# Kernel optimization log

Hardware: AMD Instinct MI355X
Metric: run time of the kernel (lower is better)

## Reference

```python
import jax, jax.numpy as jnp
import numpy as np
import math

E = 2048; H = 16; NOPE = 128; ROPE = 64; VH = 128; C = 512; QR = 1536
DR = 2; BASE = 10000.0; LR = 4  # hypernet low_rank -> C//4 = 128
B = 2; S = 2048


def _ln(x, g, b):
    m = jnp.mean(x, axis=-1, keepdims=True)
    v = jnp.mean((x - m) ** 2, axis=-1, keepdims=True)
    return (x - m) / jnp.sqrt(v + 1e-5) * g + b


def _rope(x, sin, cos):
    # interleaved rotary: x[..., 0::2], x[..., 1::2]
    x1 = x[..., 0::2]
    x2 = x[..., 1::2]
    out = jnp.stack([x1 * cos - x2 * sin, x1 * sin + x2 * cos], axis=-1)
    return out.reshape(x.shape)


def _sincos(pos, dim):
    inv = BASE ** (-jnp.arange(0, dim, 2, dtype=jnp.float32) / dim)
    ang = pos[:, None] * inv  # [S, dim//2]
    return jnp.sin(ang), jnp.cos(ang)


def _pe(T, d):
    # sinusoidal positional encoding [T, d]
    pos = jnp.arange(T, dtype=jnp.float32)[:, None]
    div = jnp.exp(jnp.arange(0, d, 2, dtype=jnp.float32) * (-math.log(10000.0) / d))
    pe = jnp.zeros((T, d))
    pe = pe.at[:, 0::2].set(jnp.sin(pos * div))
    pe = pe.at[:, 1::2].set(jnp.cos(pos * div))
    return pe


def _forward(query, key, value, wq_a, q_ln_g, q_ln_b, wq_b, wkv_a, kv_ln_g,
             kv_ln_b, wkv_b, wo, fc_c_w, fc_c_b, fc_p_w, fc_p_b, pos_scale):
    B_, S_, _ = query.shape
    # LoRA query path
    ql = _ln(query @ wq_a.T, q_ln_g, q_ln_b)                 # [B,S,QR]
    q = (ql @ wq_b.T).reshape(B_, S_, H, NOPE + ROPE)
    q_nope, q_pe = q[..., :NOPE], q[..., NOPE:]
    # positions: start_pos = key_len - 1 (prefill entering incremental path)
    start = S_ - 1
    pos = jnp.arange(start, start + S_, dtype=jnp.float32)
    sin, cos = _sincos(pos, ROPE)                            # [S, ROPE//2]
    q_pe = _rope(q_pe, sin[None, :, None, :], cos[None, :, None, :])
    # KV latent path
    kvf = key @ wkv_a.T                                      # [B,S,C+ROPE]
    kv, k_pe = kvf[..., :C], kvf[..., C:]
    k_pe = _rope(k_pe, sin[None, :, :], cos[None, :, :])     # [B,S,ROPE]
    kvn = _ln(kv, kv_ln_g, kv_ln_b)                          # [B,S,C]
    # HyperNetwork temporal compression: W [B, t, T]
    T = S_
    t = math.ceil(T / DR)
    Cpe = _pe(t, C)                                          # [t, C]
    C2 = Cpe @ fc_c_w.T + fc_c_b                             # [t, C//LR]
    P2 = kvn @ fc_p_w.T + fc_p_b                             # [B,T,C//LR]
    W = jax.nn.sigmoid(jnp.einsum('tr,bTr->btT', C2, P2))    # [B,t,T]
    # chunk mask: compressed slot r gathers tokens in its down_rate chunk
    zm = (jnp.arange(T)[None, :] // DR == jnp.arange(t)[:, None]).astype(kvn.dtype)
    prev_kv = jnp.einsum('btT,bTc->btc', W * zm[None], kvn)  # [B,t,C]
    idx = list(range(DR - 1, T, DR))
    if T - 1 not in idx:
        idx.append(T - 1)
    prev_kpe = k_pe[:, np.array(idx)]                        # [B,t,ROPE]
    # LoRA-absorbed attention
    wkvb = wkv_b.reshape(H, NOPE + VH, C)
    qn = jnp.einsum('bshd,hdc->bshc', q_nope, wkvb[:, :NOPE])
    content = jnp.einsum('bshc,btc->bsht', qn, prev_kv)
    # decoupled (normalized) rope scores
    qpe_n = q_pe / jnp.maximum(jnp.linalg.norm(q_pe, axis=-1, keepdims=True), 1e-12)
    kpe_n = prev_kpe / jnp.maximum(jnp.linalg.norm(prev_kpe, axis=-1, keepdims=True), 1e-12)
    pscore = jnp.einsum('bshr,btr->bsht', qpe_n, kpe_n)
    scores = (content + pos_scale * pscore) * ((NOPE + ROPE) ** -0.5)
    attn = jax.nn.softmax(scores, axis=-1)                   # [B,S,H,t]
    x = jnp.einsum('bsht,btc->bshc', attn, prev_kv)
    x = jnp.einsum('bshc,hdc->bshd', x, wkvb[:, NOPE:])      # value up-proj
    return x.reshape(B_, S_, H * VH) @ wo.T


def setup_inputs() -> dict:
    key = jax.random.key(0)
    ks = jax.random.split(key, 16)
    s = 0.02
    return {
        'query': jax.random.normal(ks[0], (B, S, E), jnp.float32),
        'key': jax.random.normal(ks[1], (B, S, E), jnp.float32),
        'value': jax.random.normal(ks[2], (B, S, E), jnp.float32),
        'wq_a': jax.random.normal(ks[3], (QR, E), jnp.float32) * s,
        'q_ln_g': jnp.ones((QR,), jnp.float32),
        'q_ln_b': jnp.zeros((QR,), jnp.float32),
        'wq_b': jax.random.normal(ks[4], (H * (NOPE + ROPE), QR), jnp.float32) * s,
        'wkv_a': jax.random.normal(ks[5], (C + ROPE, E), jnp.float32) * s,
        'kv_ln_g': jnp.ones((C,), jnp.float32),
        'kv_ln_b': jnp.zeros((C,), jnp.float32),
        'wkv_b': jax.random.normal(ks[6], (H * (NOPE + VH), C), jnp.float32) * s,
        'wo': jax.random.normal(ks[7], (E, H * VH), jnp.float32) * s,
        'fc_c_w': jax.random.normal(ks[8], (C // LR, C), jnp.float32) * s,
        'fc_c_b': jnp.zeros((C // LR,), jnp.float32),
        'fc_p_w': jax.random.normal(ks[9], (C // LR, C), jnp.float32) * s,
        'fc_p_b': jnp.zeros((C // LR,), jnp.float32),
        'pos_scale': jnp.asarray(1.0, jnp.float32),
    }


def reference(query, key, value, wq_a, q_ln_g, q_ln_b, wq_b, wkv_a, kv_ln_g,
              kv_ln_b, wkv_b, wo, fc_c_w, fc_c_b, fc_p_w, fc_p_b, pos_scale):
    return _forward(query, key, value, wq_a, q_ln_g, q_ln_b, wq_b, wkv_a,
                    kv_ln_g, kv_ln_b, wkv_b, wo, fc_c_w, fc_c_b, fc_p_w,
                    fc_p_b, pos_scale)
```

## Files before the change

### kernel.cpp

```cpp
#include <hip/hip_runtime.h>
#include <math.h>

#define S_ 2048
#define B_ 2
#define H_ 16
#define E_ 2048
#define QR_ 1536
#define NOPE_ 128
#define ROPE_ 64
#define C_ 512
#define VH_ 128
#define T_ 1024
#define LN1E4 9.210340371976184f
#define SCALE_ 0.07216878364870323f

typedef _Float16 half8 __attribute__((ext_vector_type(8)));
typedef _Float16 half4 __attribute__((ext_vector_type(4)));
typedef __fp16 fp16x2 __attribute__((ext_vector_type(2)));
typedef float floatx4 __attribute__((ext_vector_type(4)));
#define MFMA16(a, b, c) __builtin_amdgcn_mfma_f32_16x16x32_f16(a, b, c, 0, 0, 0)

__device__ __forceinline__ void gload16(const _Float16* g, _Float16* l) {
  __builtin_amdgcn_global_load_lds(
      (__attribute__((address_space(1))) const void*)g,
      (__attribute__((address_space(3))) void*)l, 16, 0, 0);
}

__device__ __forceinline__ int xcd_swizzle(int orig, int nwg) {
  int q8 = nwg >> 3, r8 = nwg & 7, xcd = orig & 7, base = orig >> 3;
  return (xcd < r8 ? xcd * (q8 + 1) : r8 * (q8 + 1) + (xcd - r8) * q8) + base;
}

__global__ __launch_bounds__(256) void conv_all(
    const float* __restrict__ q, const float* __restrict__ k,
    const float* __restrict__ wqa, const float* __restrict__ wqb,
    const float* __restrict__ wkva, const float* __restrict__ wo,
    const float* __restrict__ fcc, const float* __restrict__ fcp,
    const float* __restrict__ wkvb,
    _Float16* q16, _Float16* k16, _Float16* wqa16, _Float16* wqb16,
    _Float16* wkva16, _Float16* wo16, _Float16* fcc16, _Float16* fcp16,
    _Float16* W1c, _Float16* W2c)
{
  size_t i = (size_t)blockIdx.x * 256 + threadIdx.x;
  if (i >= 3768320) {
    bool isW1 = i < 3899392;
    size_t j = i - (isW1 ? 3768320 : 3899392);
    int cch = j & 63, hd = (int)(j >> 6);
    int hh = hd >> 7, dd = hd & 127;
    const float* src = wkvb + ((size_t)(hh * 256 + (isW1 ? 0 : 128) + dd)) * 512 + cch * 8;
    float sc = isW1 ? SCALE_ : 1.f;
    float4 a = *(const float4*)src;
    float4 b = *(const float4*)(src + 4);
    half8 h = {(_Float16)(a.x * sc), (_Float16)(a.y * sc), (_Float16)(a.z * sc),
               (_Float16)(a.w * sc), (_Float16)(b.x * sc), (_Float16)(b.y * sc),
               (_Float16)(b.z * sc), (_Float16)(b.w * sc)};
    *(half8*)((isW1 ? W1c : W2c) + j * 8) = h;
    return;
  }
  const float* in; _Float16* out; size_t off;
  if      (i < 1048576) { in = q;    out = q16;    off = i; }
  else if (i < 2097152) { in = k;    out = k16;    off = i - 1048576; }
  else if (i < 2490368) { in = wqa;  out = wqa16;  off = i - 2097152; }
  else if (i < 3080192) { in = wqb;  out = wqb16;  off = i - 2490368; }
  else if (i < 3227648) { in = wkva; out = wkva16; off = i - 3080192; }
  else if (i < 3751936) { in = wo;   out = wo16;   off = i - 3227648; }
  else if (i < 3760128) { in = fcc;  out = fcc16;  off = i - 3751936; }
  else                  { in = fcp;  out = fcp16;  off = i - 3760128; }
  float4 a = ((const float4*)in)[2 * off];
  float4 b = ((const float4*)in)[2 * off + 1];
  half8 h = {(_Float16)a.x, (_Float16)a.y, (_Float16)a.z, (_Float16)a.w,
             (_Float16)b.x, (_Float16)b.y, (_Float16)b.z, (_Float16)b.w};
  *(half8*)(out + 8 * off) = h;
}

template<bool OUT16, bool NB, bool BIAS, bool TRANSC, bool DUAL = false>
__global__ __launch_bounds__(256) void gemm16(
    const _Float16* __restrict__ A, const _Float16* __restrict__ Bm,
    const float* __restrict__ bias, const float* __restrict__ bias2,
    float* __restrict__ Cf, _Float16* __restrict__ Ch,
    int N, int K, int lda, int ldb, int ldc,
    long sAb, long sAh, long sBb, long sBh, long sCb, long sCh)
{
  __shared__ __align__(16) _Float16 Asl[2][128 * 64];
  __shared__ __align__(16) _Float16 Bsl[2][128 * 64];
  int mode = 0;
  if (DUAL) {
    int zz = blockIdx.z;
    mode = zz >> 5;
    int z2 = zz & 31;
    int zb2 = z2 >> 4, zh2 = z2 & 15;
    A += (size_t)zb2 * sAb;
    const _Float16* Bsel = mode ? (const _Float16*)bias2 : Bm;
    Bm = Bsel + (size_t)zh2 * (128 * C_);
    if (mode) Ch = ((_Float16*)Cf) + ((size_t)(zb2 * H_ + zh2) * 128) * T_;
    else      Ch += ((size_t)(zb2 * H_ + zh2) * T_) * 192;
  } else {
    const int z = blockIdx.z, zb = z >> 4, zh = z & 15;
    A  += (size_t)zb * sAb + (size_t)zh * sAh;
    Bm += (size_t)zb * sBb + (size_t)zh * sBh;
    if (OUT16) Ch += (size_t)zb * sCb + (size_t)zh * sCh;
    else       Cf += (size_t)zb * sCb + (size_t)zh * sCh;
  }
  const int gx = gridDim.x;
  const int nwg = gx * gridDim.y;
  const int f = xcd_swizzle(blockIdx.y * gx + blockIdx.x, nwg);
  const int bm = (f / gx) * 128, bn = (f % gx) * 128;
  const int tid = threadIdx.x;
  const int w = tid >> 6, lane = tid & 63, l15 = lane & 15, g = lane >> 4;
  const int wm = (w >> 1) * 64, wn = (w & 1) * 64;
  const int srow = w * 32 + (lane >> 3);
  const int sch  = (lane & 7) ^ (lane >> 3);
  floatx4 acc[4][4];
  #pragma unroll
  for (int i = 0; i < 4; ++i)
    #pragma unroll
    for (int j = 0; j < 4; ++j) acc[i][j] = (floatx4){0.f, 0.f, 0.f, 0.f};

  auto STAGE = [&](int buf, int k0) {
    _Float16* al = &Asl[buf][w * 2048];
    _Float16* bl = &Bsl[buf][w * 2048];
    #pragma unroll
    for (int i = 0; i < 4; ++i)
      gload16(A + (size_t)(bm + srow + i * 8) * lda + k0 + sch * 8, al + i * 512);
    #pragma unroll
    for (int i = 0; i < 4; ++i)
      gload16(Bm + (size_t)(bn + srow + i * 8) * ldb + k0 + sch * 8, bl + i * 512);
  };

  STAGE(0, 0);
  int cur = 0;
  const int nIter = K >> 6;
  for (int it = 0; it < nIter; ++it) {
    const bool pf = (it + 1 < nIter);
    if (pf) STAGE(cur ^ 1, (it + 1) << 6);
    if (pf) asm volatile("s_waitcnt vmcnt(8)" ::: "memory");
    else    asm volatile("s_waitcnt vmcnt(0)" ::: "memory");
    __builtin_amdgcn_sched_barrier(0);
    __builtin_amdgcn_s_barrier();
    __builtin_amdgcn_sched_barrier(0);
    #pragma unroll
    for (int kk = 0; kk < 2; ++kk) {
      half8 af[4], bf[4];
      const int sw = ((kk * 4 + g) ^ (l15 & 7)) * 8;
      #pragma unroll
      for (int i = 0; i < 4; ++i) {
        af[i] = *(const half8*)&Asl[cur][(wm + i * 16 + l15) * 64 + sw];
        bf[i] = *(const half8*)&Bsl[cur][(wn + i * 16 + l15) * 64 + sw];
      }
      #pragma unroll
      for (int i = 0; i < 4; ++i)
        #pragma unroll
        for (int j = 0; j < 4; ++j)
          acc[i][j] = MFMA16(af[i], bf[j], acc[i][j]);
    }
    asm volatile("s_waitcnt lgkmcnt(0)" ::: "memory");
    __builtin_amdgcn_sched_barrier(0);
    __builtin_amdgcn_s_barrier();
    __builtin_amdgcn_sched_barrier(0);
    cur ^= 1;
  }

  if (DUAL) {
    if (mode) {
      #pragma unroll
      for (int i = 0; i < 4; ++i)
        #pragma unroll
        for (int j = 0; j < 4; ++j) {
          int row = bm + wm + i * 16 + g * 4;
          int col = wn + j * 16 + l15;
          half4 v = {(_Float16)acc[i][j][0], (_Float16)acc[i][j][1],
                     (_Float16)acc[i][j][2], (_Float16)acc[i][j][3]};
          *(half4*)(Ch + (size_t)col * T_ + row) = v;
        }
    } else {
      #pragma unroll
      for (int i = 0; i < 4; ++i)
        #pragma unroll
        for (int j = 0; j < 4; ++j)
          #pragma unroll
          for (int r = 0; r < 4; ++r) {
            int row = bm + wm + i * 16 + g * 4 + r;
            int col = wn + j * 16 + l15;
            Ch[(size_t)row * 192 + col] = (_Float16)acc[i][j][r];
          }
    }
  } else if (TRANSC) {
    #pragma unroll
    for (int i = 0; i < 4; ++i)
      #pragma unroll
      for (int j = 0; j < 4; ++j) {
        int row = bm + wm + i * 16 + g * 4;
        int col = bn + wn + j * 16 + l15;
        half4 v = {(_Float16)acc[i][j][0], (_Float16)acc[i][j][1],
                   (_Float16)acc[i][j][2], (_Float16)acc[i][j][3]};
        *(half4*)(Ch + (size_t)col * ldc + row) = v;
      }
  } else {
    #pragma unroll
    for (int i = 0; i < 4; ++i)
      #pragma unroll
      for (int j = 0; j < 4; ++j)
        #pragma unroll
        for (int r = 0; r < 4; ++r) {
          int row = bm + wm + i * 16 + g * 4 + r;
          int col = bn + wn + j * 16 + l15;
          if (!NB || col < N) {
            float v = acc[i][j][r];
            if (BIAS) v += (col < 128) ? bias[col] : bias2[col - 128];
            if (OUT16) Ch[(size_t)row * ldc + col] = (_Float16)v;
            else       Cf[(size_t)row * ldc + col] = v;
          }
        }
  }
}

struct GTask {
  const _Float16* A; const _Float16* B; _Float16* C;
  const float* b1; const float* b2;
  int gx, N, K, lda, ldb, ldc;
};

__global__ __launch_bounds__(256) void gemm_pair(GTask ta, GTask tb, int n0, int n1)
{
  __shared__ __align__(16) _Float16 Asl[2][128 * 64];
  __shared__ __align__(16) _Float16 Bsl[2][128 * 64];
  const bool second = blockIdx.x >= (unsigned)n0;
  GTask t = second ? tb : ta;
  const int fid = second ? blockIdx.x - n0 : blockIdx.x;
  const int nwg = second ? n1 : n0;
  const int f = xcd_swizzle(fid, nwg);
  const int bm = (f / t.gx) * 128, bn = (f % t.gx) * 128;
  const int tid = threadIdx.x;
  const int w = tid >> 6, lane = tid & 63, l15 = lane & 15, g = lane >> 4;
  const int wm = (w >> 1) * 64, wn = (w & 1) * 64;
  const int srow = w * 32 + (lane >> 3);
  const int sch  = (lane & 7) ^ (lane >> 3);
  floatx4 acc[4][4];
  #pragma unroll
  for (int i = 0; i < 4; ++i)
    #pragma unroll
    for (int j = 0; j < 4; ++j) acc[i][j] = (floatx4){0.f, 0.f, 0.f, 0.f};

  auto STAGE = [&](int buf, int k0) {
    _Float16* al = &Asl[buf][w * 2048];
    _Float16* bl = &Bsl[buf][w * 2048];
    #pragma unroll
    for (int i = 0; i < 4; ++i)
      gload16(t.A + (size_t)(bm + srow + i * 8) * t.lda + k0 + sch * 8, al + i * 512);
    #pragma unroll
    for (int i = 0; i < 4; ++i)
      gload16(t.B + (size_t)(bn + srow + i * 8) * t.ldb + k0 + sch * 8, bl + i * 512);
  };

  STAGE(0, 0);
  int cur = 0;
  const int nIter = t.K >> 6;
  for (int it = 0; it < nIter; ++it) {
    const bool pf = (it + 1 < nIter);
    if (pf) STAGE(cur ^ 1, (it + 1) << 6);
    if (pf) asm volatile("s_waitcnt vmcnt(8)" ::: "memory");
    else    asm volatile("s_waitcnt vmcnt(0)" ::: "memory");
    __builtin_amdgcn_sched_barrier(0);
    __builtin_amdgcn_s_barrier();
    __builtin_amdgcn_sched_barrier(0);
    #pragma unroll
    for (int kk = 0; kk < 2; ++kk) {
      half8 af[4], bf[4];
      const int sw = ((kk * 4 + g) ^ (l15 & 7)) * 8;
      #pragma unroll
      for (int i = 0; i < 4; ++i) {
        af[i] = *(const half8*)&Asl[cur][(wm + i * 16 + l15) * 64 + sw];
        bf[i] = *(const half8*)&Bsl[cur][(wn + i * 16 + l15) * 64 + sw];
      }
      #pragma unroll
      for (int i = 0; i < 4; ++i)
        #pragma unroll
        for (int j = 0; j < 4; ++j)
          acc[i][j] = MFMA16(af[i], bf[j], acc[i][j]);
    }
    asm volatile("s_waitcnt lgkmcnt(0)" ::: "memory");
    __builtin_amdgcn_sched_barrier(0);
    __builtin_amdgcn_s_barrier();
    __builtin_amdgcn_sched_barrier(0);
    cur ^= 1;
  }
  #pragma unroll
  for (int i = 0; i < 4; ++i)
    #pragma unroll
    for (int j = 0; j < 4; ++j)
      #pragma unroll
      for (int r = 0; r < 4; ++r) {
        int row = bm + wm + i * 16 + g * 4 + r;
        int col = bn + wn + j * 16 + l15;
        if (col < t.N) {
          float v = acc[i][j][r];
          if (t.b1) v += (col < 128) ? t.b1[col] : t.b2[col - 128];
          t.C[(size_t)row * t.ldc + col] = (_Float16)v;
        }
      }
}

__global__ __launch_bounds__(256) void fused_ln(
    _Float16* __restrict__ ql16, const _Float16* __restrict__ kvf16,
    _Float16* __restrict__ kvnA,
    const float* __restrict__ qg, const float* __restrict__ qb,
    const float* __restrict__ kg, const float* __restrict__ kb,
    _Float16* __restrict__ keff, _Float16* __restrict__ Cpe16)
{
  __shared__ float rs[4], rs2[4];
  int bid = blockIdx.x;
  const int tid = threadIdx.x;
  const int lane = tid & 63, w = tid >> 6;
  if (bid < 8192) {
    const bool isQ = bid < 4096;
    const int row = isQ ? bid : bid - 4096;
    const _Float16* x = isQ ? ql16 + (size_t)row * 1536 : kvf16 + (size_t)row * 576;
    _Float16* o = isQ ? ql16 + (size_t)row * 1536 : kvnA + (size_t)row * 512;
    const float* g_ = isQ ? qg : kg;
    const float* b_ = isQ ? qb : kb;
    const int L = isQ ? 1536 : 512;
    float s = 0.f, s2 = 0.f;
    for (int i = tid; i < L; i += 256) {
      float v = (float)x[i]; s += v; s2 += v * v;
    }
    #pragma unroll
    for (int off = 32; off; off >>= 1) {
      s  += __shfl_xor(s, off, 64);
      s2 += __shfl_xor(s2, off, 64);
    }
    if (lane == 0) { rs[w] = s; rs2[w] = s2; }
    __syncthreads();
    s  = rs[0] + rs[1] + rs[2] + rs[3];
    s2 = rs2[0] + rs2[1] + rs2[2] + rs2[3];
    float mean = s / L;
    float var = s2 / L - mean * mean;
    float inv = rsqrtf(var + 1e-5f);
    for (int i = tid; i < L; i += 256)
      o[i] = (_Float16)(((float)x[i] - mean) * inv * g_[i] + b_[i]);
    return;
  }
  bid -= 8192;
  if (bid < 512) {
    int u = bid * 4 + w;
    int t = u & (T_ - 1), b = u >> 10;
    const int srow = 2 * t + 1;
    const _Float16* p = kvf16 + ((size_t)(b * S_ + srow)) * 576 + C_;
    float o1 = 0.f, o2 = 0.f;
    if (lane < 32) {
      float invf = expf(-(float)lane * (LN1E4 / 32.f));
      float ang = (float)(S_ - 1 + srow) * invf;
      float sn, cs; sincosf(ang, &sn, &cs);
      float x1 = (float)p[2 * lane], x2 = (float)p[2 * lane + 1];
      o1 = x1 * cs - x2 * sn;
      o2 = x1 * sn + x2 * cs;
    }
    float ss = o1 * o1 + o2 * o2;
    #pragma unroll
    for (int off = 32; off; off >>= 1) ss += __shfl_xor(ss, off, 64);
    float nrm = fmaxf(sqrtf(ss), 1e-12f);
    if (lane < 32) {
      _Float16 h1 = (_Float16)(o1 / nrm), h2 = (_Float16)(o2 / nrm);
      #pragma unroll
      for (int h = 0; h < H_; ++h) {
        _Float16* o = keff + ((size_t)((b * H_ + h) * T_) + t) * 192 + NOPE_;
        o[2 * lane] = h1; o[2 * lane + 1] = h2;
      }
    }
    return;
  }
  bid -= 512;
  {
    const int t = bid;
    float dv = expf(-(float)(2 * tid) * (LN1E4 / 512.f));
    float ang = (float)t * dv;
    float sn, cs; sincosf(ang, &sn, &cs);
    Cpe16[(size_t)t * C_ + 2 * tid]     = (_Float16)sn;
    Cpe16[(size_t)t * C_ + 2 * tid + 1] = (_Float16)cs;
  }
}

__global__ __launch_bounds__(256) void fused_rq_gate(
    _Float16* __restrict__ qb16, const float* __restrict__ ps_ptr,
    const _Float16* __restrict__ Ccat, const _Float16* __restrict__ kvnA,
    _Float16* __restrict__ pkv16)
{
  int bid = blockIdx.x;
  const int tid = threadIdx.x;
  const int lane = tid & 63, w = tid >> 6;
  if (bid < 4096) {
    const int row = bid;
    const int s = row & (S_ - 1);
    float sn = 0.f, cs = 0.f;
    if (lane < 32) {
      float invf = expf(-(float)lane * (LN1E4 / 32.f));
      float ang = (float)(S_ - 1 + s) * invf;
      sincosf(ang, &sn, &cs);
    }
    const float psc = ps_ptr[0] * SCALE_;
    #pragma unroll
    for (int hh = 0; hh < 4; ++hh) {
      const int h = w + hh * 4;
      _Float16* p = qb16 + (size_t)row * 3072 + h * 192 + NOPE_;
      float o1 = 0.f, o2 = 0.f;
      if (lane < 32) {
        float x1 = (float)p[2 * lane], x2 = (float)p[2 * lane + 1];
        o1 = x1 * cs - x2 * sn;
        o2 = x1 * sn + x2 * cs;
      }
      float ss = o1 * o1 + o2 * o2;
      #pragma unroll
      for (int off = 32; off; off >>= 1) ss += __shfl_xor(ss, off, 64);
      float inv = psc / fmaxf(sqrtf(ss), 1e-12f);
      if (lane < 32) {
        p[2 * lane]     = (_Float16)(o1 * inv);
        p[2 * lane + 1] = (_Float16)(o2 * inv);
      }
    }
    return;
  }
  bid -= 4096;
  {
    int u = bid * 4 + w;
    int t = u & (T_ - 1), b = u >> 10;
    const int j = lane;
    const _Float16* c2 = Ccat + (size_t)t * 256;
    const _Float16* p0 = Ccat + (size_t)(1024 + b * S_ + 2 * t) * 256 + 128;
    const _Float16* p1 = p0 + 256;
    float d0 = (float)c2[j] * (float)p0[j] + (float)c2[j + 64] * (float)p0[j + 64];
    float d1 = (float)c2[j] * (float)p1[j] + (float)c2[j + 64] * (float)p1[j + 64];
    #pragma unroll
    for (int off = 32; off; off >>= 1) {
      d0 += __shfl_xor(d0, off, 64);
      d1 += __shfl_xor(d1, off, 64);
    }
    float w0 = 1.f / (1.f + expf(-d0));
    float w1 = 1.f / (1.f + expf(-d1));
    const _Float16* k0 = kvnA + ((size_t)(b * S_ + 2 * t)) * C_;
    const _Float16* k1 = k0 + C_;
    _Float16* o = pkv16 + ((size_t)(b * T_ + t)) * C_;
    #pragma unroll
    for (int it = 0; it < 2; ++it) {
      int c = j * 4 + it * 256;
      half4 a = *(const half4*)(k0 + c);
      half4 bb = *(const half4*)(k1 + c);
      half4 r;
      #pragma unroll
      for (int uu = 0; uu < 4; ++uu)
        r[uu] = (_Float16)(w0 * (float)a[uu] + w1 * (float)bb[uu]);
      *(half4*)(o + c) = r;
    }
  }
}

__global__ __launch_bounds__(256, 2) void attn_flash(
    const _Float16* __restrict__ qb16, const _Float16* __restrict__ keff,
    const _Float16* __restrict__ vT, _Float16* __restrict__ x216)
{
  __shared__ __align__(16) _Float16 K_lds[2][64 * 192];
  __shared__ __align__(16) _Float16 V_lds[2][128 * 64];
  const int f = xcd_swizzle(blockIdx.x, 1024);
  const int st = f & 31, h = (f >> 5) & 15, b = f >> 9;
  const int tid = threadIdx.x, w = tid >> 6, lane = tid & 63;
  const int l15 = lane & 15, g = lane >> 4, l7 = lane & 7;
  const int rq = b * S_ + st * 64 + w * 16;
  const _Float16* qrow = qb16 + (size_t)(rq + l15) * 3072 + h * 192;
  half8 qB[6];
  #pragma unroll
  for (int kk = 0; kk < 6; ++kk) qB[kk] = *(const half8*)(qrow + kk * 32 + g * 8);
  floatx4 O[8];
  #pragma unroll
  for (int i = 0; i < 8; ++i) O[i] = (floatx4){0.f, 0.f, 0.f, 0.f};
  float m = -3e38f, l = 0.f;
  const _Float16* kb = keff + (size_t)(b * H_ + h) * T_ * 192;
  const _Float16* vb = vT   + (size_t)(b * H_ + h) * 128 * T_;

  int ksrc[6], ksw[6], vsrc[4], vsw[4];
  #pragma unroll
  for (int p = 0; p < 6; ++p) {
    int c = tid + p * 256;
    int r = c / 24, dc = c % 24;
    ksrc[p] = r * 192 + dc * 8;
    ksw[p]  = r * 192 + ((dc ^ (r & 7)) * 8);
  }
  #pragma unroll
  for (int p = 0; p < 4; ++p) {
    int c = tid + p * 256;
    int r = c >> 3, dc = c & 7;
    vsrc[p] = r * T_ + dc * 8;
    vsw[p]  = r * 64 + ((dc ^ (r & 7)) * 8);
  }
  int kswr[6], vswr[2];
  #pragma unroll
  for (int kk = 0; kk < 6; ++kk) kswr[kk] = ((kk * 4 + g) ^ l7) * 8;
  #pragma unroll
  for (int kc = 0; kc < 2; ++kc) vswr[kc] = ((kc * 4 + g) ^ l7) * 8;

  half8 kreg[6], vreg[4];
  #pragma unroll
  for (int p = 0; p < 6; ++p) kreg[p] = *(const half8*)(kb + ksrc[p]);
  #pragma unroll
  for (int p = 0; p < 4; ++p) vreg[p] = *(const half8*)(vb + vsrc[p]);
  #pragma unroll
  for (int p = 0; p < 6; ++p) *(half8*)&K_lds[0][ksw[p]] = kreg[p];
  #pragma unroll
  for (int p = 0; p < 4; ++p) *(half8*)&V_lds[0][vsw[p]] = vreg[p];
  __syncthreads();

  const int srcA = l15 + ((g & 1) << 5);
  const int srcB = srcA + 16;
  const bool hi = (g >> 1) != 0;

  int cur = 0;
  for (int kt = 0; kt < 16; ++kt) {
    if (kt < 15) {
      const int t1 = (kt + 1) * 64;
      #pragma unroll
      for (int p = 0; p < 6; ++p)
        kreg[p] = *(const half8*)(kb + (size_t)t1 * 192 + ksrc[p]);
      #pragma unroll
      for (int p = 0; p < 4; ++p)
        vreg[p] = *(const half8*)(vb + t1 + vsrc[p]);
    }
    floatx4 sc[4];
    #pragma unroll
    for (int i = 0; i < 4; ++i) sc[i] = (floatx4){0.f, 0.f, 0.f, 0.f};
    __builtin_amdgcn_s_setprio(1);
    #pragma unroll
    for (int kk = 0; kk < 6; ++kk)
      #pragma unroll
      for (int ct = 0; ct < 4; ++ct)
        sc[ct] = MFMA16(
            *(const half8*)&K_lds[cur][(ct * 16 + l15) * 192 + kswr[kk]],
            qB[kk], sc[ct]);
    __builtin_amdgcn_s_setprio(0);
    float pm = sc[0][0];
    #pragma unroll
    for (int ct = 0; ct < 4; ++ct)
      #pragma unroll
      for (int r = 0; r < 4; ++r) pm = fmaxf(pm, sc[ct][r]);
    pm = fmaxf(pm, __shfl_xor(pm, 16, 64));
    pm = fmaxf(pm, __shfl_xor(pm, 32, 64));
    int ok = pm <= m + 8.f;
    if (!__all(ok)) {
      float mn = fmaxf(m, pm);
      float sf = __expf(m - mn);
      m = mn; l *= sf;
      float sfO[4];
      #pragma unroll
      for (int r = 0; r < 4; ++r) sfO[r] = __shfl(sf, g * 4 + r, 64);
      #pragma unroll
      for (int cc = 0; cc < 8; ++cc) {
        O[cc][0] *= sfO[0]; O[cc][1] *= sfO[1];
        O[cc][2] *= sfO[2]; O[cc][3] *= sfO[3];
      }
    }
    float rs = 0.f;
    #pragma unroll
    for (int ct = 0; ct < 4; ++ct)
      #pragma unroll
      for (int r = 0; r < 4; ++r) {
        float e = __expf(sc[ct][r] - m);
        sc[ct][r] = e; rs += e;
      }
    rs += __shfl_xor(rs, 16, 64);
    rs += __shfl_xor(rs, 32, 64);
    l += rs;
    unsigned pk[4][2];
    #pragma unroll
    for (int ct = 0; ct < 4; ++ct) {
      union { fp16x2 h; unsigned u; } c0, c1;
      c0.h = __builtin_amdgcn_cvt_pkrtz(sc[ct][0], sc[ct][1]);
      c1.h = __builtin_amdgcn_cvt_pkrtz(sc[ct][2], sc[ct][3]);
      pk[ct][0] = c0.u; pk[ct][1] = c1.u;
    }
    __builtin_amdgcn_s_setprio(1);
    #pragma unroll
    for (int kc = 0; kc < 2; ++kc) {
      unsigned a0 = __shfl((int)pk[2 * kc][0], srcA, 64);
      unsigned b0 = __shfl((int)pk[2 * kc + 1][0], srcA, 64);
      unsigned a1 = __shfl((int)pk[2 * kc][1], srcA, 64);
      unsigned b1 = __shfl((int)pk[2 * kc + 1][1], srcA, 64);
      unsigned a2 = __shfl((int)pk[2 * kc][0], srcB, 64);
      unsigned b2 = __shfl((int)pk[2 * kc + 1][0], srcB, 64);
      unsigned a3 = __shfl((int)pk[2 * kc][1], srcB, 64);
      unsigned b3 = __shfl((int)pk[2 * kc + 1][1], srcB, 64);
      union { unsigned u[4]; half8 h; } pa;
      pa.u[0] = hi ? b0 : a0;
      pa.u[1] = hi ? b1 : a1;
      pa.u[2] = hi ? b2 : a2;
      pa.u[3] = hi ? b3 : a3;
      #pragma unroll
      for (int cc = 0; cc < 8; ++cc)
        O[cc] = MFMA16(pa.h,
            *(const half8*)&V_lds[cur][(cc * 16 + l15) * 64 + vswr[kc]], O[cc]);
    }
    __builtin_amdgcn_s_setprio(0);
    if (kt < 15) {
      #pragma unroll
      for (int p = 0; p < 6; ++p) *(half8*)&K_lds[cur ^ 1][ksw[p]] = kreg[p];
      #pragma unroll
      for (int p = 0; p < 4; ++p) *(half8*)&V_lds[cur ^ 1][vsw[p]] = vreg[p];
      __syncthreads();
      cur ^= 1;
    }
  }
  float il = 1.f / l;
  float ilO[4];
  #pragma unroll
  for (int r = 0; r < 4; ++r) ilO[r] = __shfl(il, g * 4 + r, 64);
  #pragma unroll
  for (int cc = 0; cc < 8; ++cc)
    #pragma unroll
    for (int r = 0; r < 4; ++r)
      x216[(size_t)(rq + g * 4 + r) * 2048 + h * 128 + cc * 16 + l15] =
          (_Float16)(O[cc][r] * ilO[r]);
}

extern "C" void kernel_launch(void* const* d_in, const int* in_sizes, int n_in,
                              void* d_out, int out_size, void* d_ws, size_t ws_size,
                              hipStream_t stream)
{
  (void)in_sizes; (void)n_in; (void)out_size; (void)ws_size;
  const float* query  = (const float*)d_in[0];
  const float* key    = (const float*)d_in[1];
  const float* wq_a   = (const float*)d_in[3];
  const float* q_ln_g = (const float*)d_in[4];
  const float* q_ln_b = (const float*)d_in[5];
  const float* wq_b   = (const float*)d_in[6];
  const float* wkv_a  = (const float*)d_in[7];
  const float* kv_ln_g= (const float*)d_in[8];
  const float* kv_ln_b= (const float*)d_in[9];
  const float* wkvb   = (const float*)d_in[10];
  const float* wo     = (const float*)d_in[11];
  const float* fc_c_w = (const float*)d_in[12];
  const float* fc_c_b = (const float*)d_in[13];
  const float* fc_p_w = (const float*)d_in[14];
  const float* fc_p_b = (const float*)d_in[15];
  const float* ps     = (const float*)d_in[16];
  float* out = (float*)d_out;

  const int M = B_ * S_;
  _Float16* hws   = (_Float16*)d_ws;
  _Float16* q16   = hws;
  _Float16* key16 = q16   + (size_t)8388608;
  _Float16* wqa16 = key16 + (size_t)8388608;
  _Float16* wqb16 = wqa16 + (size_t)3145728;
  _Float16* wkva16= wqb16 + (size_t)4718592;
  _Float16* wo16  = wkva16+ (size_t)1179648;
  _Float16* ql16  = wo16  + (size_t)4194304;
  _Float16* qb16  = ql16  + (size_t)6291456;
  _Float16* kvf16 = qb16  + (size_t)12582912;
  _Float16* kvn16 = kvf16 + (size_t)2359296;
  _Float16* fcc16 = kvn16 + (size_t)2097152;
  _Float16* fcp16 = fcc16 + (size_t)65536;
  _Float16* W1c   = fcp16 + (size_t)65536;
  _Float16* W2c   = W1c   + (size_t)1048576;
  _Float16* x216  = q16;
  _Float16* keff  = key16;
  _Float16* Cpe16 = q16;
  _Float16* kvnA  = q16 + (size_t)524288;
  _Float16* Ccat  = wqa16;
  _Float16* pkv16 = wkva16;
  _Float16* vT    = ql16;

  conv_all<<<15744, 256, 0, stream>>>(query, key, wq_a, wq_b, wkv_a, wo, fc_c_w, fc_p_w,
                                      wkvb, q16, key16, wqa16, wqb16, wkva16, wo16,
                                      fcc16, fcp16, W1c, W2c);
  {
    GTask ta = {q16,   wqa16,  ql16,  nullptr, nullptr, 12, QR_, E_, E_, E_, QR_};
    GTask tb = {key16, wkva16, kvf16, nullptr, nullptr, 5,  576, E_, E_, E_, 576};
    gemm_pair<<<544, 256, 0, stream>>>(ta, tb, 384, 160);
  }
  fused_ln<<<9728, 256, 0, stream>>>(ql16, kvf16, kvnA, q_ln_g, q_ln_b,
                                     kv_ln_g, kv_ln_b, keff, Cpe16);
  {
    GTask ta = {ql16,  wqb16, qb16, nullptr, nullptr, 24, 3072, QR_, QR_, QR_, 3072};
    GTask tb = {Cpe16, fcc16, Ccat, fc_c_b,  fc_p_b,  2,  256,  C_,  C_,  C_,  256};
    gemm_pair<<<848, 256, 0, stream>>>(ta, tb, 768, 80);
  }
  fused_rq_gate<<<4608, 256, 0, stream>>>(qb16, ps, Ccat, kvnA, pkv16);
  gemm16<true,false,false,false,true><<<dim3(1, T_/128, 64), 256, 0, stream>>>(
      pkv16, W1c, nullptr, (const float*)W2c, (float*)vT, keff,
      128, C_, C_, C_, 192, (long)T_*C_, 0L, 0L, 0L, 0L, 0L);
  attn_flash<<<dim3(1024), 256, 0, stream>>>(qb16, keff, vT, x216);
  gemm16<false,false,false,false><<<dim3(E_/128, M/128), 256, 0, stream>>>(
      x216, wo16, nullptr, nullptr, out, nullptr, E_, E_, E_, E_, E_, 0,0,0,0,0,0);
}
```

Measured before the change: 322.1 us.

## Overlap deferred weight conversions with first GEMM pair launch

Splits the fp32-to-fp16 conversion kernel so only the inputs needed by the first GEMM pair (query, key, wq_a, wkv_a) are converted up front. The remaining weight conversions (wq_b, wo, fc weights, wkv_b split/scale) are appended as extra blocks to the first gemm_pair launch, so they can run on CUs left idle by the 544 GEMM tiles. The aim is to shorten the serial conversion phase and fill the GEMM's underutilized GPU. The cost is a larger grid and a branch in the GEMM kernel. The conversion blocks also share the kernel's LDS allocation, which may limit how many of them run at once.

```diff
diff --git a/kernel.cpp b/kernel.cpp
--- a/kernel.cpp
+++ b/kernel.cpp
@@ -31,41 +31,17 @@
   return (xcd < r8 ? xcd * (q8 + 1) : r8 * (q8 + 1) + (xcd - r8) * q8) + base;
 }
 
-__global__ __launch_bounds__(256) void conv_all(
+__global__ __launch_bounds__(256) void conv_a(
     const float* __restrict__ q, const float* __restrict__ k,
-    const float* __restrict__ wqa, const float* __restrict__ wqb,
-    const float* __restrict__ wkva, const float* __restrict__ wo,
-    const float* __restrict__ fcc, const float* __restrict__ fcp,
-    const float* __restrict__ wkvb,
-    _Float16* q16, _Float16* k16, _Float16* wqa16, _Float16* wqb16,
-    _Float16* wkva16, _Float16* wo16, _Float16* fcc16, _Float16* fcp16,
-    _Float16* W1c, _Float16* W2c)
+    const float* __restrict__ wqa, const float* __restrict__ wkva,
+    _Float16* q16, _Float16* k16, _Float16* wqa16, _Float16* wkva16)
 {
   size_t i = (size_t)blockIdx.x * 256 + threadIdx.x;
-  if (i >= 3768320) {
-    bool isW1 = i < 3899392;
-    size_t j = i - (isW1 ? 3768320 : 3899392);
-    int cch = j & 63, hd = (int)(j >> 6);
-    int hh = hd >> 7, dd = hd & 127;
-    const float* src = wkvb + ((size_t)(hh * 256 + (isW1 ? 0 : 128) + dd)) * 512 + cch * 8;
-    float sc = isW1 ? SCALE_ : 1.f;
-    float4 a = *(const float4*)src;
-    float4 b = *(const float4*)(src + 4);
-    half8 h = {(_Float16)(a.x * sc), (_Float16)(a.y * sc), (_Float16)(a.z * sc),
-               (_Float16)(a.w * sc), (_Float16)(b.x * sc), (_Float16)(b.y * sc),
-               (_Float16)(b.z * sc), (_Float16)(b.w * sc)};
-    *(half8*)((isW1 ? W1c : W2c) + j * 8) = h;
-    return;
-  }
   const float* in; _Float16* out; size_t off;
   if      (i < 1048576) { in = q;    out = q16;    off = i; }
   else if (i < 2097152) { in = k;    out = k16;    off = i - 1048576; }
   else if (i < 2490368) { in = wqa;  out = wqa16;  off = i - 2097152; }
-  else if (i < 3080192) { in = wqb;  out = wqb16;  off = i - 2490368; }
-  else if (i < 3227648) { in = wkva; out = wkva16; off = i - 3080192; }
-  else if (i < 3751936) { in = wo;   out = wo16;   off = i - 3227648; }
-  else if (i < 3760128) { in = fcc;  out = fcc16;  off = i - 3751936; }
-  else                  { in = fcp;  out = fcp16;  off = i - 3760128; }
+  else                  { in = wkva; out = wkva16; off = i - 2490368; }
   float4 a = ((const float4*)in)[2 * off];
   float4 b = ((const float4*)in)[2 * off + 1];
   half8 h = {(_Float16)a.x, (_Float16)a.y, (_Float16)a.z, (_Float16)a.w,
@@ -219,12 +195,51 @@
   const float* b1; const float* b2;
   int gx, N, K, lda, ldb, ldc;
 };
-
-__global__ __launch_bounds__(256) void gemm_pair(GTask ta, GTask tb, int n0, int n1)
+struct CTask {
+  const float* wqb; const float* wo; const float* fcc; const float* fcp;
+  const float* wkvb;
+  _Float16* wqb16; _Float16* wo16; _Float16* fcc16; _Float16* fcp16;
+  _Float16* W1c; _Float16* W2c;
+};
+
+__global__ __launch_bounds__(256) void gemm_pair(GTask ta, GTask tb, CTask tc,
+                                                 int n0, int n1)
 {
   __shared__ __align__(16) _Float16 Asl[2][128 * 64];
   __shared__ __align__(16) _Float16 Bsl[2][128 * 64];
-  const bool second = blockIdx.x >= (unsigned)n0;
+  if ((int)blockIdx.x >= n0 + n1) {
+    size_t j = (size_t)(blockIdx.x - n0 - n1) * 256 + threadIdx.x;
+    const float* in; _Float16* out; size_t off; float sc = 1.f;
+    if (j < 589824)       { in = tc.wqb; out = tc.wqb16; off = j; }
+    else if (j < 1114112) { in = tc.wo;  out = tc.wo16;  off = j - 589824; }
+    else if (j < 1122304) { in = tc.fcc; out = tc.fcc16; off = j - 1114112; }
+    else if (j < 1130496) { in = tc.fcp; out = tc.fcp16; off = j - 1122304; }
+    else {
+      size_t j2 = j - 1130496;
+      bool isW1 = j2 < 131072;
+      size_t jj = isW1 ? j2 : j2 - 131072;
+      int cch = jj & 63, hd = (int)(jj >> 6);
+      int hh = hd >> 7, dd = hd & 127;
+      in = tc.wkvb + ((size_t)(hh * 256 + (isW1 ? 0 : 128) + dd)) * 512 + cch * 8
+           - 0;
+      out = (isW1 ? tc.W1c : tc.W2c) + jj * 8;
+      sc = isW1 ? SCALE_ : 1.f;
+      float4 a = *(const float4*)in;
+      float4 b = *(const float4*)(in + 4);
+      half8 h = {(_Float16)(a.x * sc), (_Float16)(a.y * sc), (_Float16)(a.z * sc),
+                 (_Float16)(a.w * sc), (_Float16)(b.x * sc), (_Float16)(b.y * sc),
+                 (_Float16)(b.z * sc), (_Float16)(b.w * sc)};
+      *(half8*)out = h;
+      return;
+    }
+    float4 a = ((const float4*)in)[2 * off];
+    float4 b = ((const float4*)in)[2 * off + 1];
+    half8 h = {(_Float16)a.x, (_Float16)a.y, (_Float16)a.z, (_Float16)a.w,
+               (_Float16)b.x, (_Float16)b.y, (_Float16)b.z, (_Float16)b.w};
+    *(half8*)(out + 8 * off) = h;
+    return;
+  }
+  const bool second = (int)blockIdx.x >= n0;
   GTask t = second ? tb : ta;
   const int fid = second ? blockIdx.x - n0 : blockIdx.x;
   const int nwg = second ? n1 : n0;
@@ -663,20 +678,22 @@
   _Float16* pkv16 = wkva16;
   _Float16* vT    = ql16;
 
-  conv_all<<<15744, 256, 0, stream>>>(query, key, wq_a, wq_b, wkv_a, wo, fc_c_w, fc_p_w,
-                                      wkvb, q16, key16, wqa16, wqb16, wkva16, wo16,
-                                      fcc16, fcp16, W1c, W2c);
+  conv_a<<<10304, 256, 0, stream>>>(query, key, wq_a, wkv_a,
+                                    q16, key16, wqa16, wkva16);
   {
     GTask ta = {q16,   wqa16,  ql16,  nullptr, nullptr, 12, QR_, E_, E_, E_, QR_};
     GTask tb = {key16, wkva16, kvf16, nullptr, nullptr, 5,  576, E_, E_, E_, 576};
-    gemm_pair<<<544, 256, 0, stream>>>(ta, tb, 384, 160);
+    CTask tc = {wq_b, wo, fc_c_w, fc_p_w, wkvb,
+                wqb16, wo16, fcc16, fcp16, W1c, W2c};
+    gemm_pair<<<544 + 5440, 256, 0, stream>>>(ta, tb, tc, 384, 160);
   }
   fused_ln<<<9728, 256, 0, stream>>>(ql16, kvf16, kvnA, q_ln_g, q_ln_b,
                                      kv_ln_g, kv_ln_b, keff, Cpe16);
   {
     GTask ta = {ql16,  wqb16, qb16, nullptr, nullptr, 24, 3072, QR_, QR_, QR_, 3072};
     GTask tb = {Cpe16, fcc16, Ccat, fc_c_b,  fc_p_b,  2,  256,  C_,  C_,  C_,  256};
-    gemm_pair<<<848, 256, 0, stream>>>(ta, tb, 768, 80);
+    CTask tc = {};
+    gemm_pair<<<848, 256, 0, stream>>>(ta, tb, tc, 768, 80);
   }
   fused_rq_gate<<<4608, 256, 0, stream>>>(qb16, ps, Ccat, kvnA, pkv16);
   gemm16<true,false,false,false,true><<<dim3(1, T_/128, 64), 256, 0, stream>>>(
```

Measured after the change: 313.1 us. 2.8% less time.
